# Kernel tuning notes

Hardware: AMD Instinct MI355X
Metric: run time of the kernel (lower is better)

Reference implementation:

```python
import jax, jax.numpy as jnp
import numpy as np

B, LQ, LK, D, H, DK, DV = 8, 1024, 1024, 512, 8, 64, 64
EPS = 1e-14          # K.epsilon()**2 with default K.epsilon()=1e-7
MASK_VALUE = -1e30   # default mask_value in call()


def setup_inputs() -> dict:
    key = jax.random.key(0)
    ks = jax.random.split(key, 7)
    query = jax.random.normal(ks[0], (B, LQ, D), jnp.float32)
    key_t = jax.random.normal(ks[1], (B, LK, D), jnp.float32)
    value = jax.random.normal(ks[2], (B, LK, D), jnp.float32)
    mask = jax.random.randint(ks[3], (B, LK), 0, 2).astype(jnp.float32)
    glorot = np.sqrt(2.0 / (D + DK)).astype(np.float32)
    Wq = jax.random.normal(ks[4], (H, D, DK), jnp.float32) * glorot
    Wk = jax.random.normal(ks[5], (H, D, DK), jnp.float32) * glorot
    Wv = jax.random.normal(ks[6], (H, D, DV), jnp.float32) * glorot
    gamma = jnp.ones((1,), jnp.float32)
    beta = jnp.zeros((1,), jnp.float32)
    return {"query": query, "key": key_t, "value": value, "mask": mask,
            "Wq": Wq, "Wk": Wk, "Wv": Wv, "gamma": gamma, "beta": beta}


def reference(query, key, value, mask, Wq, Wk, Wv, gamma, beta):
    # Per-head projections (the original's Python loop over heads, vectorized).
    q = jnp.einsum('bqd,hde->bhqe', query, Wq)   # [B,H,LQ,DK]
    k = jnp.einsum('bkd,hde->bhke', key, Wk)     # [B,H,LK,DK]
    v = jnp.einsum('bkd,hde->bhke', value, Wv)   # [B,H,LK,DV]
    # NOTE: no 1/sqrt(dk) scaling, faithful to the source.
    A = jnp.einsum('bhqe,bhke->bhqk', q, k)      # [B,H,LQ,LK]
    m = mask[:, None, None, :]                    # [B,1,1,LK] broadcast over heads & queries
    A = m * A + (1.0 - m) * MASK_VALUE
    A = jax.nn.softmax(A, axis=-1)
    o = jnp.einsum('bhqk,bhke->bhqe', A, v)      # [B,H,LQ,DV]
    conc = o.transpose(0, 2, 1, 3).reshape(B, LQ, H * DV)  # concat heads
    # Scalar-affine layernorm over the concatenated feature dim.
    mean = jnp.mean(conc, axis=-1, keepdims=True)
    var = jnp.mean(jnp.square(conc - mean), axis=-1, keepdims=True)
    x = (conc - mean) / jnp.sqrt(var + EPS)
    return x * gamma[0] + beta[0]
```

## Files before the change

### kernel.cpp

```cpp
#include <hip/hip_runtime.h>
#include <math.h>

#define NB 8
#define NLQ 1024
#define NLK 1024
#define ND 512
#define NH 8
#define MASKV -1e30f
#define LOG2E 1.44269504088896f
#define SHIFT2 32.0f

typedef unsigned short ushort_t;
typedef __attribute__((ext_vector_type(8))) _Float16 f16x8;
typedef __attribute__((ext_vector_type(8))) short bf16x8;
typedef __attribute__((ext_vector_type(16))) float f32x16;

__device__ __forceinline__ ushort_t f2h_bits(float f) {
    union { _Float16 h; ushort_t u; } v; v.h = (_Float16)f;
    return v.u;
}
__device__ __forceinline__ ushort_t f2bf(float f) {
    union { float f; unsigned u; } v; v.f = f;
    unsigned r = v.u + 0x7fffu + ((v.u >> 16) & 1u);
    return (ushort_t)(r >> 16);
}
__device__ __forceinline__ void gload16(const ushort_t* g, ushort_t* l) {
    __builtin_amdgcn_global_load_lds(
        (const __attribute__((address_space(1))) void*)g,
        (__attribute__((address_space(3))) void*)l, 16, 0, 0);
}
__device__ __forceinline__ unsigned pack_bf16_trunc(float p0, float p1) {
    return __builtin_amdgcn_perm(__float_as_uint(p1), __float_as_uint(p0),
                                 0x07060302u);
}

__global__ __launch_bounds__(256) void wsplit_kernel(
    const float* __restrict__ Wq, const float* __restrict__ Wk, const float* __restrict__ Wv,
    ushort_t* __restrict__ oq, ushort_t* __restrict__ ok, ushort_t* __restrict__ ov) {
    __shared__ float T[64][65];
    const int d0 = blockIdx.x * 64;
    const int h  = blockIdx.y;
    const int t  = blockIdx.z;
    const float* W = (t == 0) ? Wq : (t == 1) ? Wk : Wv;
    ushort_t* oh = (t == 0) ? oq : (t == 1) ? ok : ov;
    const int tid = threadIdx.x;
#pragma unroll
    for (int i = 0; i < 4; i++) {
        int r = (tid >> 4) + i * 16;
        int c = (tid & 15) * 4;
        float4 v = *(const float4*)&W[((size_t)h * ND + d0 + r) * 64 + c];
        *(float4*)&T[r][c] = v;
    }
    __syncthreads();
    const int e = tid & 63;
    const int dg = tid >> 6;
    ushort_t hs[16];
#pragma unroll
    for (int dd = 0; dd < 16; dd++) hs[dd] = f2h_bits(T[dg * 16 + dd][e]);
    size_t base = ((size_t)h * 64 + e) * ND + d0 + dg * 16;
#pragma unroll
    for (int c = 0; c < 2; c++) {
        uint4 wh;
        wh.x = (unsigned)hs[8*c+0] | ((unsigned)hs[8*c+1] << 16);
        wh.y = (unsigned)hs[8*c+2] | ((unsigned)hs[8*c+3] << 16);
        wh.z = (unsigned)hs[8*c+4] | ((unsigned)hs[8*c+5] << 16);
        wh.w = (unsigned)hs[8*c+6] | ((unsigned)hs[8*c+7] << 16);
        *(uint4*)&oh[base + 8 * c] = wh;
    }
}

__global__ __launch_bounds__(256, 3) void proj_gemm_kernel(
    const float* __restrict__ Xq, const float* __restrict__ Xk,
    const float* __restrict__ Xv, const ushort_t* __restrict__ Wbase,
    ushort_t* __restrict__ Obase) {
    __shared__ ushort_t S[24960];
    ushort_t* const sA  = S;
    ushort_t* const sB0 = S + 8320;
    ushort_t* const sB1 = S + 16640;

    const int bid   = blockIdx.x;
    const int y     = bid / 192;
    const int mglob = bid % 192;
    const int t  = mglob >> 6;
    const int b  = (mglob >> 3) & 7;
    const int l0 = (mglob & 7) * 128;

    const int tid  = threadIdx.x;
    const int wave = tid >> 6;
    const int lane = tid & 63;
    const int l31  = lane & 31;
    const int hib  = lane >> 5;
    const int wr = wave >> 1, wc = wave & 1;

    const float* Xt = (t == 0) ? Xq : (t == 1) ? Xk : Xv;
    const float* gx = Xt + ((size_t)b * NLQ + l0) * ND;
    const ushort_t* gwt = Wbase + (size_t)t * ((size_t)NH * 64 * ND)
                        + (size_t)y * 128 * ND;
    ushort_t* out = Obase + (size_t)t * ((size_t)NB * NH * NLQ * 64);

    const int srow = lane >> 3;
    const int schk = (lane & 7) ^ srow;

    float4 ax[4][2];
    auto aload = [&](int d0) {
#pragma unroll
        for (int j = 0; j < 4; j++) {
            int row = (j * 4 + wave) * 8 + srow;
            const float* p = gx + (size_t)row * ND + d0 + schk * 8;
            ax[j][0] = *(const float4*)p;
            ax[j][1] = *(const float4*)(p + 4);
        }
    };
    auto awrite = [&]() {
#pragma unroll
        for (int j = 0; j < 4; j++) {
            int u = j * 4 + wave;
            uint4 hv;
            hv.x = (unsigned)f2h_bits(ax[j][0].x) | ((unsigned)f2h_bits(ax[j][0].y) << 16);
            hv.y = (unsigned)f2h_bits(ax[j][0].z) | ((unsigned)f2h_bits(ax[j][0].w) << 16);
            hv.z = (unsigned)f2h_bits(ax[j][1].x) | ((unsigned)f2h_bits(ax[j][1].y) << 16);
            hv.w = (unsigned)f2h_bits(ax[j][1].z) | ((unsigned)f2h_bits(ax[j][1].w) << 16);
            *(uint4*)(sA + u * 520 + lane * 8) = hv;
        }
    };
    auto bstage = [&](ushort_t* dst, int d0) {
#pragma unroll
        for (int j = 0; j < 4; j++) {
            int u = j * 4 + wave;
            int row = u * 8 + srow;
            gload16(gwt + (size_t)row * ND + d0 + schk * 8, dst + u * 520);
        }
    };

    f32x16 acc00, acc01, acc10, acc11;
#pragma unroll
    for (int i = 0; i < 16; i++) { acc00[i] = 0.f; acc01[i] = 0.f;
                                   acc10[i] = 0.f; acc11[i] = 0.f; }

    const int ga  = wr * 8 + (l31 >> 3);
    const int gb  = wc * 8 + (l31 >> 3);
    const int ro  = (l31 & 7) * 64;
    const int swz = l31 & 7;

    aload(0);
    awrite();
    bstage(sB0, 0);
    asm volatile("s_waitcnt vmcnt(0) lgkmcnt(0)" ::: "memory");
    __builtin_amdgcn_sched_barrier(0);
    __builtin_amdgcn_s_barrier();
    __builtin_amdgcn_sched_barrier(0);

    ushort_t* sBc = sB0;
    ushort_t* sBn = sB1;
#pragma unroll
    for (int kc = 0; kc < 8; kc++) {
        if (kc < 7) aload((kc + 1) * 64);
        f16x8 a0[4], a1[4];
#pragma unroll
        for (int c = 0; c < 4; c++) {
            const int pc = ((2 * c + hib) ^ swz) * 8;
            a0[c] = *(const f16x8*)&sA[ga * 520 + ro + pc];
            a1[c] = *(const f16x8*)&sA[(ga + 4) * 520 + ro + pc];
        }
        asm volatile("s_waitcnt lgkmcnt(0)" ::: "memory");
        __builtin_amdgcn_sched_barrier(0);
        __builtin_amdgcn_s_barrier();
        __builtin_amdgcn_sched_barrier(0);
        if (kc < 7) {
            bstage(sBn, (kc + 1) * 64);
            awrite();
        }
#pragma unroll
        for (int c = 0; c < 4; c++) {
            const int pc = ((2 * c + hib) ^ swz) * 8;
            f16x8 b0 = *(const f16x8*)&sBc[gb * 520 + ro + pc];
            f16x8 b1 = *(const f16x8*)&sBc[(gb + 4) * 520 + ro + pc];
            acc00 = __builtin_amdgcn_mfma_f32_32x32x16_f16(a0[c], b0, acc00, 0, 0, 0);
            acc01 = __builtin_amdgcn_mfma_f32_32x32x16_f16(a0[c], b1, acc01, 0, 0, 0);
            acc10 = __builtin_amdgcn_mfma_f32_32x32x16_f16(a1[c], b0, acc10, 0, 0, 0);
            acc11 = __builtin_amdgcn_mfma_f32_32x32x16_f16(a1[c], b1, acc11, 0, 0, 0);
        }
        if (kc < 7) {
            asm volatile("s_waitcnt vmcnt(0) lgkmcnt(0)" ::: "memory");
            __builtin_amdgcn_sched_barrier(0);
            __builtin_amdgcn_s_barrier();
            __builtin_amdgcn_sched_barrier(0);
        }
        ushort_t* tmp = sBc; sBc = sBn; sBn = tmp;
    }

    if (t < 2) {
        const float scale = (t == 0) ? LOG2E : 1.f;
#pragma unroll
        for (int mi = 0; mi < 2; mi++) {
#pragma unroll
            for (int ni = 0; ni < 2; ni++) {
                const f32x16& a = (mi == 0) ? (ni == 0 ? acc00 : acc01)
                                            : (ni == 0 ? acc10 : acc11);
                int nglob = y * 128 + wc * 64 + ni * 32 + l31;
                int hh = nglob >> 6, e = nglob & 63;
                size_t obase = (((size_t)b * NH + hh) * NLQ + l0) * 64 + e;
#pragma unroll
                for (int r = 0; r < 16; r++) {
                    int l = wr * 64 + mi * 32 + (r & 3) + 8 * (r >> 2) + 4 * hib;
                    out[obase + (size_t)l * 64] = f2h_bits(a[r] * scale);
                }
            }
        }
    } else {
        __syncthreads();
        ushort_t (*T)[130] = (ushort_t(*)[130])S;
#pragma unroll
        for (int mi = 0; mi < 2; mi++) {
#pragma unroll
            for (int ni = 0; ni < 2; ni++) {
                const f32x16& a = (mi == 0) ? (ni == 0 ? acc00 : acc01)
                                            : (ni == 0 ? acc10 : acc11);
                int n_loc = wc * 64 + ni * 32 + l31;
#pragma unroll
                for (int r = 0; r < 16; r++) {
                    int l = wr * 64 + mi * 32 + (r & 3) + 8 * (r >> 2) + 4 * hib;
                    T[n_loc][l] = f2bf(a[r]);
                }
            }
        }
        __syncthreads();
        const int n_loc = tid >> 1;
        const int half  = tid & 1;
        const int hh = n_loc >> 6, e = n_loc & 63;
        size_t obase = (((size_t)b * NH + y * 2 + hh) * 64 + e) * NLK
                     + l0 + half * 64;
        const ushort_t* src = &T[n_loc][half * 64];
#pragma unroll
        for (int c2 = 0; c2 < 8; c2++)
            *(uint4*)&out[obase + c2 * 8] = *(const uint4*)&src[c2 * 8];
    }
}

__global__ __launch_bounds__(512, 2) void attn_kernel(
    const ushort_t* __restrict__ Qf, const ushort_t* __restrict__ Kf,
    const ushort_t* __restrict__ Vt, const float* __restrict__ maskp,
    float* __restrict__ Op) {
    __shared__ ushort_t sK[2][4160];
    __shared__ ushort_t sV[2][4160];
    __shared__ float sBias[1024];

    const int idx = blockIdx.x;
    const int bh_i = idx & 63;
    const int qc  = idx >> 6;
    const int b = bh_i >> 3, h = bh_i & 7;
    const size_t bh = (size_t)b * NH + h;

    const int tid  = threadIdx.x;
    const int wave = tid >> 6;
    const int lane = tid & 63;
    const int l31  = lane & 31;
    const int hib  = lane >> 5;
    const int q = qc * 256 + wave * 32 + l31;
    const int sw = l31 & 7;

    if (tid < 256) {
        const float* mrow = maskp + ((size_t)b << 10);
        float4 m0 = *(const float4*)&mrow[tid * 4];
        float4 bi;
        bi.x = (m0.x > 0.5f) ? -SHIFT2 : MASKV;
        bi.y = (m0.y > 0.5f) ? -SHIFT2 : MASKV;
        bi.z = (m0.z > 0.5f) ? -SHIFT2 : MASKV;
        bi.w = (m0.w > 0.5f) ? -SHIFT2 : MASKV;
        *(float4*)&sBias[tid * 4] = bi;
    }

    f16x8 qh[4];
    {
        const ushort_t* ph = Qf + (bh * NLQ + q) * 64 + hib * 8;
#pragma unroll
        for (int c = 0; c < 4; c++) qh[c] = *(const f16x8*)(ph + c * 16);
    }

    const int srow = lane >> 3;
    const int schk = (lane & 7) ^ srow;

    auto stage = [&](int buf, int k0) {
#pragma unroll
        for (int n = 0; n < 2; n++) {
            int u = wave + n * 8;
            if (u < 8) {
                int row = u * 8 + srow;
                int key = (row & ~12) | ((row & 4) << 1) | ((row & 8) >> 1);
                gload16(Kf + ((bh << 10) + k0 + key) * 64 + schk * 8,
                        sK[buf] + u * 520);
            } else {
                int u8 = u - 8;
                int row = u8 * 8 + srow;
                gload16(Vt + ((bh << 6) + row) * NLK + k0 + schk * 8,
                        sV[buf] + u8 * 520);
            }
        }
    };

    f32x16 O0, O1;
#pragma unroll
    for (int i = 0; i < 16; i++) { O0[i] = 0.f; O1[i] = 0.f; }
    float lrun = 0.f;

    const int rp0 = (l31 >> 3) * 520 + (l31 & 7) * 64;
    const int rp1 = rp0 + 4 * 520;

    stage(0, 0);
    __syncthreads();
    int cur = 0;

    for (int t = 0; t < 16; t++) {
        const int k0 = t << 6;
        if (t < 15) stage(cur ^ 1, k0 + 64);

        f32x16 S0, S1;
#pragma unroll
        for (int g = 0; g < 4; g++) {
            const int kb = k0 + 16 * (g >> 1) + 8 * hib + 4 * (g & 1);
            float4 b0 = *(const float4*)&sBias[kb];
            float4 b1 = *(const float4*)&sBias[kb + 32];
            S0[4 * g + 0] = b0.x; S0[4 * g + 1] = b0.y;
            S0[4 * g + 2] = b0.z; S0[4 * g + 3] = b0.w;
            S1[4 * g + 0] = b1.x; S1[4 * g + 1] = b1.y;
            S1[4 * g + 2] = b1.z; S1[4 * g + 3] = b1.w;
        }
        __builtin_amdgcn_s_setprio(1);
#pragma unroll
        for (int c = 0; c < 4; c++) {
            const int pc = ((2 * c + hib) ^ sw) * 8;
            f16x8 a0 = *(const f16x8*)&sK[cur][rp0 + pc];
            f16x8 a1 = *(const f16x8*)&sK[cur][rp1 + pc];
            S0 = __builtin_amdgcn_mfma_f32_32x32x16_f16(a0, qh[c], S0, 0, 0, 0);
            S1 = __builtin_amdgcn_mfma_f32_32x32x16_f16(a1, qh[c], S1, 0, 0, 0);
        }
        __builtin_amdgcn_s_setprio(0);

        unsigned pq[8][2];
#pragma unroll
        for (int g = 0; g < 8; g++) {
            float p0, p1, p2, p3;
            if (g < 4) {
                p0 = __builtin_amdgcn_exp2f(S0[4*g+0]);
                p1 = __builtin_amdgcn_exp2f(S0[4*g+1]);
                p2 = __builtin_amdgcn_exp2f(S0[4*g+2]);
                p3 = __builtin_amdgcn_exp2f(S0[4*g+3]);
            } else {
                p0 = __builtin_amdgcn_exp2f(S1[4*(g-4)+0]);
                p1 = __builtin_amdgcn_exp2f(S1[4*(g-4)+1]);
                p2 = __builtin_amdgcn_exp2f(S1[4*(g-4)+2]);
                p3 = __builtin_amdgcn_exp2f(S1[4*(g-4)+3]);
            }
            lrun += (p0 + p1) + (p2 + p3);
            pq[g][0] = pack_bf16_trunc(p0, p1);
            pq[g][1] = pack_bf16_trunc(p2, p3);
        }

        __builtin_amdgcn_s_setprio(1);
#pragma unroll
        for (int c = 0; c < 4; c++) {
            union { unsigned u[4]; bf16x8 v; } pf;
            pf.u[0] = pq[2 * c][0];     pf.u[1] = pq[2 * c][1];
            pf.u[2] = pq[2 * c + 1][0]; pf.u[3] = pq[2 * c + 1][1];
            const int pc = ((2 * c + hib) ^ sw) * 8;
            bf16x8 v0 = *(const bf16x8*)&sV[cur][rp0 + pc];
            bf16x8 v1 = *(const bf16x8*)&sV[cur][rp1 + pc];
            O0 = __builtin_amdgcn_mfma_f32_32x32x16_bf16(v0, pf.v, O0, 0, 0, 0);
            O1 = __builtin_amdgcn_mfma_f32_32x32x16_bf16(v1, pf.v, O1, 0, 0, 0);
        }
        __builtin_amdgcn_s_setprio(0);
        __syncthreads();
        cur ^= 1;
    }

    lrun += __shfl_xor(lrun, 32);
    const float linv = 1.f / lrun;
    float* obase = Op + ((size_t)(b * NLQ + q)) * (NH * 64) + h * 64;
#pragma unroll
    for (int me = 0; me < 2; me++) {
#pragma unroll
        for (int g = 0; g < 4; g++) {
            int e0 = me * 32 + 8 * g + 4 * hib;
            float4 o;
            if (me == 0) {
                o.x = O0[4 * g + 0] * linv; o.y = O0[4 * g + 1] * linv;
                o.z = O0[4 * g + 2] * linv; o.w = O0[4 * g + 3] * linv;
            } else {
                o.x = O1[4 * g + 0] * linv; o.y = O1[4 * g + 1] * linv;
                o.z = O1[4 * g + 2] * linv; o.w = O1[4 * g + 3] * linv;
            }
            *(float4*)&obase[e0] = o;
        }
    }
}

__global__ __launch_bounds__(256) void ln_kernel(const float* __restrict__ X,
                                                 const float* __restrict__ gamma,
                                                 const float* __restrict__ beta,
                                                 float* __restrict__ out) {
    const int row = blockIdx.x * 4 + (threadIdx.x >> 6);
    const int lane = threadIdx.x & 63;
    const float* x = &X[(size_t)row * 512];
    float4 v0 = *(const float4*)&x[lane * 8];
    float4 v1 = *(const float4*)&x[lane * 8 + 4];
    float sum = v0.x + v0.y + v0.z + v0.w + v1.x + v1.y + v1.z + v1.w;
    float sq = v0.x * v0.x + v0.y * v0.y + v0.z * v0.z + v0.w * v0.w
             + v1.x * v1.x + v1.y * v1.y + v1.z * v1.z + v1.w * v1.w;
#pragma unroll
    for (int off = 32; off > 0; off >>= 1) {
        sum += __shfl_down(sum, off);
        sq  += __shfl_down(sq, off);
    }
    sum = __shfl(sum, 0);
    sq  = __shfl(sq, 0);
    const float mean = sum * (1.f / 512.f);
    const float var = sq * (1.f / 512.f) - mean * mean;
    const float rstd = rsqrtf(var + 1e-14f);
    const float g = gamma[0], be = beta[0];
    float* o = &out[(size_t)row * 512];
    float4 r0, r1;
    r0.x = (v0.x - mean) * rstd * g + be;  r0.y = (v0.y - mean) * rstd * g + be;
    r0.z = (v0.z - mean) * rstd * g + be;  r0.w = (v0.w - mean) * rstd * g + be;
    r1.x = (v1.x - mean) * rstd * g + be;  r1.y = (v1.y - mean) * rstd * g + be;
    r1.z = (v1.z - mean) * rstd * g + be;  r1.w = (v1.w - mean) * rstd * g + be;
    *(float4*)&o[lane * 8] = r0;
    *(float4*)&o[lane * 8 + 4] = r1;
}

extern "C" void kernel_launch(void* const* d_in, const int* in_sizes, int n_in,
                              void* d_out, int out_size, void* d_ws, size_t ws_size,
                              hipStream_t stream) {
    const float* query = (const float*)d_in[0];
    const float* key_t = (const float*)d_in[1];
    const float* value = (const float*)d_in[2];
    const float* mask  = (const float*)d_in[3];
    const float* Wq    = (const float*)d_in[4];
    const float* Wk    = (const float*)d_in[5];
    const float* Wv    = (const float*)d_in[6];
    const float* gamma = (const float*)d_in[7];
    const float* beta  = (const float*)d_in[8];
    float* out = (float*)d_out;

    const size_t A = (size_t)NB * NLQ * ND;
    const size_t WS = (size_t)NH * 64 * ND;
    ushort_t* Qf = (ushort_t*)d_ws;
    ushort_t* Kf = Qf + A;
    ushort_t* Vt = Qf + 2 * A;
    ushort_t* Wt = Qf + 3 * A;

    wsplit_kernel<<<dim3(ND / 64, NH, 3), 256, 0, stream>>>(
        Wq, Wk, Wv, Wt, Wt + WS, Wt + 2 * WS);

    proj_gemm_kernel<<<768, 256, 0, stream>>>(
        query, key_t, value, Wt, Qf);

    attn_kernel<<<256, 512, 0, stream>>>(Qf, Kf, Vt, mask, out);

    ln_kernel<<<(NB * NLQ) / 4, 256, 0, stream>>>(out, gamma, beta, out);
}
```

Baseline: 157.8 us.

## Split attention KV range across two wave groups per block and merge partials

Doubles the attention block to 1024 threads, where two wave groups each process half of the key/value sequence with their own double-buffered LDS tiles. Partial O accumulators and row sums from the second group are reduced through shared memory before normalization and store. This raises waves per CU since the grid only has one block per CU, trading extra LDS use and a final reduction step.

```diff
diff --git a/kernel.cpp b/kernel.cpp
--- a/kernel.cpp
+++ b/kernel.cpp
@@ -237,12 +237,11 @@
     }
 }
 
-__global__ __launch_bounds__(512, 2) void attn_kernel(
+__global__ __launch_bounds__(1024, 1) void attn_kernel(
     const ushort_t* __restrict__ Qf, const ushort_t* __restrict__ Kf,
     const ushort_t* __restrict__ Vt, const float* __restrict__ maskp,
     float* __restrict__ Op) {
-    __shared__ ushort_t sK[2][4160];
-    __shared__ ushort_t sV[2][4160];
+    __shared__ ushort_t SMEM[33280];
     __shared__ float sBias[1024];
 
     const int idx = blockIdx.x;
@@ -251,13 +250,18 @@
     const int b = bh_i >> 3, h = bh_i & 7;
     const size_t bh = (size_t)b * NH + h;
 
-    const int tid  = threadIdx.x;
-    const int wave = tid >> 6;
-    const int lane = tid & 63;
-    const int l31  = lane & 31;
-    const int hib  = lane >> 5;
-    const int q = qc * 256 + wave * 32 + l31;
+    const int tid   = threadIdx.x;
+    const int wave  = tid >> 6;
+    const int strip = wave >> 1;
+    const int grp   = wave & 1;
+    const int lane  = tid & 63;
+    const int l31   = lane & 31;
+    const int hib   = lane >> 5;
+    const int q = qc * 256 + strip * 32 + l31;
     const int sw = l31 & 7;
+
+    auto sKp = [&](int g, int bf) { return SMEM + (g * 4 + bf * 2 + 0) * 4160; };
+    auto sVp = [&](int g, int bf) { return SMEM + (g * 4 + bf * 2 + 1) * 4160; };
 
     if (tid < 256) {
         const float* mrow = maskp + ((size_t)b << 10);
@@ -283,17 +287,17 @@
     auto stage = [&](int buf, int k0) {
 #pragma unroll
         for (int n = 0; n < 2; n++) {
-            int u = wave + n * 8;
+            int u = strip + n * 8;
             if (u < 8) {
                 int row = u * 8 + srow;
                 int key = (row & ~12) | ((row & 4) << 1) | ((row & 8) >> 1);
                 gload16(Kf + ((bh << 10) + k0 + key) * 64 + schk * 8,
-                        sK[buf] + u * 520);
+                        sKp(grp, buf) + u * 520);
             } else {
                 int u8 = u - 8;
                 int row = u8 * 8 + srow;
                 gload16(Vt + ((bh << 6) + row) * NLK + k0 + schk * 8,
-                        sV[buf] + u8 * 520);
+                        sVp(grp, buf) + u8 * 520);
             }
         }
     };
@@ -306,13 +310,13 @@
     const int rp0 = (l31 >> 3) * 520 + (l31 & 7) * 64;
     const int rp1 = rp0 + 4 * 520;
 
-    stage(0, 0);
+    stage(0, grp * 512);
     __syncthreads();
     int cur = 0;
 
-    for (int t = 0; t < 16; t++) {
-        const int k0 = t << 6;
-        if (t < 15) stage(cur ^ 1, k0 + 64);
+    for (int t = 0; t < 8; t++) {
+        const int k0 = (grp * 8 + t) << 6;
+        if (t < 7) stage(cur ^ 1, k0 + 64);
 
         f32x16 S0, S1;
 #pragma unroll
@@ -329,8 +333,8 @@
 #pragma unroll
         for (int c = 0; c < 4; c++) {
             const int pc = ((2 * c + hib) ^ sw) * 8;
-            f16x8 a0 = *(const f16x8*)&sK[cur][rp0 + pc];
-            f16x8 a1 = *(const f16x8*)&sK[cur][rp1 + pc];
+            f16x8 a0 = *(const f16x8*)&sKp(grp, cur)[rp0 + pc];
+            f16x8 a1 = *(const f16x8*)&sKp(grp, cur)[rp1 + pc];
             S0 = __builtin_amdgcn_mfma_f32_32x32x16_f16(a0, qh[c], S0, 0, 0, 0);
             S1 = __builtin_amdgcn_mfma_f32_32x32x16_f16(a1, qh[c], S1, 0, 0, 0);
         }
@@ -363,8 +367,8 @@
             pf.u[0] = pq[2 * c][0];     pf.u[1] = pq[2 * c][1];
             pf.u[2] = pq[2 * c + 1][0]; pf.u[3] = pq[2 * c + 1][1];
             const int pc = ((2 * c + hib) ^ sw) * 8;
-            bf16x8 v0 = *(const bf16x8*)&sV[cur][rp0 + pc];
-            bf16x8 v1 = *(const bf16x8*)&sV[cur][rp1 + pc];
+            bf16x8 v0 = *(const bf16x8*)&sVp(grp, cur)[rp0 + pc];
+            bf16x8 v1 = *(const bf16x8*)&sVp(grp, cur)[rp1 + pc];
             O0 = __builtin_amdgcn_mfma_f32_32x32x16_bf16(v0, pf.v, O0, 0, 0, 0);
             O1 = __builtin_amdgcn_mfma_f32_32x32x16_bf16(v1, pf.v, O1, 0, 0, 0);
         }
@@ -373,23 +377,45 @@
         cur ^= 1;
     }
 
-    lrun += __shfl_xor(lrun, 32);
-    const float linv = 1.f / lrun;
-    float* obase = Op + ((size_t)(b * NLQ + q)) * (NH * 64) + h * 64;
-#pragma unroll
-    for (int me = 0; me < 2; me++) {
-#pragma unroll
-        for (int g = 0; g < 4; g++) {
-            int e0 = me * 32 + 8 * g + 4 * hib;
-            float4 o;
-            if (me == 0) {
-                o.x = O0[4 * g + 0] * linv; o.y = O0[4 * g + 1] * linv;
-                o.z = O0[4 * g + 2] * linv; o.w = O0[4 * g + 3] * linv;
-            } else {
-                o.x = O1[4 * g + 0] * linv; o.y = O1[4 * g + 1] * linv;
-                o.z = O1[4 * g + 2] * linv; o.w = O1[4 * g + 3] * linv;
+    float* scr = (float*)SMEM;
+    float* slr = (float*)sBias;
+    if (grp == 1) {
+        float* basep = scr + strip * 2048;
+#pragma unroll
+        for (int i = 0; i < 16; i++) {
+            basep[i * 64 + lane]        = O0[i];
+            basep[(16 + i) * 64 + lane] = O1[i];
+        }
+        slr[strip * 64 + lane] = lrun;
+    }
+    __syncthreads();
+    if (grp == 0) {
+        float* basep = scr + strip * 2048;
+#pragma unroll
+        for (int i = 0; i < 16; i++) {
+            O0[i] += basep[i * 64 + lane];
+            O1[i] += basep[(16 + i) * 64 + lane];
+        }
+        lrun += slr[strip * 64 + lane];
+
+        lrun += __shfl_xor(lrun, 32);
+        const float linv = 1.f / lrun;
+        float* obase = Op + ((size_t)(b * NLQ + q)) * (NH * 64) + h * 64;
+#pragma unroll
+        for (int me = 0; me < 2; me++) {
+#pragma unroll
+            for (int g = 0; g < 4; g++) {
+                int e0 = me * 32 + 8 * g + 4 * hib;
+                float4 o;
+                if (me == 0) {
+                    o.x = O0[4 * g + 0] * linv; o.y = O0[4 * g + 1] * linv;
+                    o.z = O0[4 * g + 2] * linv; o.w = O0[4 * g + 3] * linv;
+                } else {
+                    o.x = O1[4 * g + 0] * linv; o.y = O1[4 * g + 1] * linv;
+                    o.z = O1[4 * g + 2] * linv; o.w = O1[4 * g + 3] * linv;
+                }
+                *(float4*)&obase[e0] = o;
             }
-            *(float4*)&obase[e0] = o;
         }
     }
 }
@@ -454,7 +480,7 @@
     proj_gemm_kernel<<<768, 256, 0, stream>>>(
         query, key_t, value, Wt, Qf);
 
-    attn_kernel<<<256, 512, 0, stream>>>(Qf, Kf, Vt, mask, out);
+    attn_kernel<<<256, 1024, 0, stream>>>(Qf, Kf, Vt, mask, out);
 
     ln_kernel<<<(NB * NLQ) / 4, 256, 0, stream>>>(out, gamma, beta, out);
 }
```

After: 155.2 us. Within noise of the previous version (-1.7%).
